# Kernel tuning notes

Hardware: AMD Instinct MI355X
Metric: run time of the kernel (lower is better)

The kernel has to match this reference:

```python
import jax, jax.numpy as jnp
import numpy as np

N = 200_000          # nodes (chain graph)
E = N - 1            # edges = diff structure
F = 5                # node features: [pos, vel_hist(3), cur_vel]
L = 16               # latent_size
G = 2                # globals: [time, static_param]
D = 3 * L + G        # ODE state dim = node_lat + sent_agg + recv_agg + globals
NSTEPS = 4           # fixed RK4 steps standing in for adaptive Tsit5 over t in [0,1]
DT = 0.01            # integrator dt of the physics post-processor


def setup_inputs() -> dict:
    key = jax.random.key(0)
    ks = iter(jax.random.split(key, 32))
    s = 0.1  # small init so the ODE stays well-behaved
    p = lambda shape: jax.random.normal(next(ks), shape, jnp.float32) * s
    inp = {}
    inp["nodes"] = jax.random.normal(next(ks), (N, F), jnp.float32)
    inp["edges"] = jax.random.normal(next(ks), (E, 1), jnp.float32)
    inp["g"] = jnp.zeros((G,), jnp.float32)
    inp["enc_n_w1"] = p((F, L)); inp["enc_n_b1"] = jnp.zeros((L,), jnp.float32)
    inp["enc_n_w2"] = p((L, L)); inp["enc_n_b2"] = jnp.zeros((L,), jnp.float32)
    inp["enc_e_w1"] = p((1, L)); inp["enc_e_b1"] = jnp.zeros((L,), jnp.float32)
    inp["enc_e_w2"] = p((L, L)); inp["enc_e_b2"] = jnp.zeros((L,), jnp.float32)
    inp["ode_w1"] = p((D + 1, D)); inp["ode_b1"] = jnp.zeros((D,), jnp.float32)
    inp["ode_w2"] = p((D, D)); inp["ode_b2"] = jnp.zeros((D,), jnp.float32)
    inp["node_out_w"] = p((D, L)); inp["node_out_b"] = jnp.zeros((L,), jnp.float32)
    inp["dec_n_w1"] = p((L, L)); inp["dec_n_b1"] = jnp.zeros((L,), jnp.float32)
    inp["dec_n_w2"] = p((L, L)); inp["dec_n_b2"] = jnp.zeros((L,), jnp.float32)
    inp["dec_n_w3"] = p((L, 1)); inp["dec_n_b3"] = jnp.zeros((1,), jnp.float32)
    inp["senders"] = jnp.arange(E, dtype=jnp.int32)
    inp["receivers"] = jnp.arange(1, N, dtype=jnp.int32)
    return inp


def reference(nodes, edges, g,
              enc_n_w1, enc_n_b1, enc_n_w2, enc_n_b2,
              enc_e_w1, enc_e_b1, enc_e_w2, enc_e_b2,
              ode_w1, ode_b1, ode_w2, ode_b2,
              node_out_w, node_out_b,
              dec_n_w1, dec_n_b1, dec_n_w2, dec_n_b2, dec_n_w3, dec_n_b3,
              senders, receivers):
    swish = jax.nn.swish
    n = nodes.shape[0]
    cur_pos = nodes[:, 0]
    cur_vel = nodes[:, -1]

    # --- encoder: MLP [L, L] on nodes and edges (swish, no final act) ---
    nlat = swish(nodes @ enc_n_w1 + enc_n_b1) @ enc_n_w2 + enc_n_b2   # [N, L]
    elat = swish(edges @ enc_e_w1 + enc_e_b1) @ enc_e_w2 + enc_e_b2   # [E, L]

    # --- processor (1 MP step): gather/scatter + Neural-ODE node update ---
    sent = jax.ops.segment_sum(elat, senders, num_segments=n)        # [N, L]
    recv = jax.ops.segment_sum(elat, receivers, num_segments=n)      # [N, L]
    gb = jnp.broadcast_to(g, (n, g.shape[0]))                        # [N, G]
    y0 = jnp.concatenate([nlat, sent, recv, gb], axis=1)             # [N, D]

    def f(t, y):  # derivative net: relu MLP on concat(y, t)
        inp = jnp.concatenate([y, jnp.full((y.shape[0], 1), t, y.dtype)], axis=1)
        return jax.nn.relu(inp @ ode_w1 + ode_b1) @ ode_w2 + ode_b2

    h = jnp.float32(1.0 / NSTEPS)

    def step(carry, _):
        y, t = carry
        k1 = f(t, y)
        k2 = f(t + 0.5 * h, y + 0.5 * h * k1)
        k3 = f(t + 0.5 * h, y + 0.5 * h * k2)
        k4 = f(t + h, y + h * k3)
        y = y + (h / 6.0) * (k1 + 2.0 * k2 + 2.0 * k3 + k4)
        return (y, t + h), None

    (yT, _), _ = jax.lax.scan(step, (y0, jnp.float32(0.0)), None, length=NSTEPS)
    nlat2 = yT @ node_out_w + node_out_b                             # [N, L]

    # --- global update: increment time ---
    g_new = jnp.concatenate([g[:1] + 1.0, g[1:]])

    # --- decoder node MLP [L, L, 1] ---
    dh = swish(nlat2 @ dec_n_w1 + dec_n_b1)
    dh = swish(dh @ dec_n_w2 + dec_n_b2)
    pred_acc = (dh @ dec_n_w3 + dec_n_b3).reshape(-1)                # [N]

    # --- semi-implicit Euler post-processor ---
    next_vel = cur_vel + pred_acc * DT
    next_pos = cur_pos + next_vel * DT
    next_nodes = jnp.column_stack([next_pos, nodes[:, 2:], next_vel, pred_acc])
    next_edges = jnp.diff(next_pos).reshape(-1, 1)
    return next_nodes, next_edges, g_new
```

## Files before the change

### kernel.cpp

```cpp
#include <hip/hip_runtime.h>

#define NN 200000
#define EE (NN - 1)
#define NSTEPS 4
#define DTC 0.01f
#define WPB 4
#define NPB 128
#define GRID 1563

typedef __attribute__((ext_vector_type(8))) _Float16 f16x8;
typedef __attribute__((ext_vector_type(2))) _Float16 f16x2;
typedef __attribute__((ext_vector_type(4))) float f32x4;

struct H4 { f16x2 a, b, c, d; };

__device__ __forceinline__ f16x2 c2h(float lo, float hi) {
    return __builtin_bit_cast(f16x2, __builtin_amdgcn_cvt_pkrtz(lo, hi));
}
__device__ __forceinline__ unsigned pk2h(float lo, float hi) {
    return __builtin_bit_cast(unsigned, __builtin_amdgcn_cvt_pkrtz(lo, hi));
}
__device__ __forceinline__ f16x8 h8(f16x2 a, f16x2 b, f16x2 c, f16x2 d) {
    H4 t{a, b, c, d};
    return __builtin_bit_cast(f16x8, t);
}
__device__ __forceinline__ f16x2 relu2(f16x2 v) {
    f16x2 r;
    asm("v_pk_max_f16 %0, %1, 0" : "=v"(r) : "v"(v));
    return r;
}
__device__ __forceinline__ float swishf(float x) { return x / (1.0f + __expf(-x)); }

__device__ __forceinline__ int permk(int k) {
    return (k & 0x23) | ((k & 4) << 2) | ((k & 0x18) >> 1);
}

__device__ __forceinline__ f16x8 setw(f16x8 v, bool cond, unsigned nw) {
    uint4 u = __builtin_bit_cast(uint4, v);
    u.w = cond ? nw : u.w;
    return __builtin_bit_cast(f16x8, u);
}

__global__ void gnode_weights(const float* __restrict__ ode_w1, const float* __restrict__ ode_b1,
                              const float* __restrict__ ode_w2, const float* __restrict__ ode_b2,
                              const float* __restrict__ enc_n_w2, const float* __restrict__ enc_e_w2,
                              const float* __restrict__ dec_n_w1, const float* __restrict__ dec_n_w2,
                              const float* __restrict__ node_out_w,
                              unsigned short* __restrict__ wg)
{
    const int b = blockIdx.x;
    const int tid = threadIdx.x;
    if (b < 8) {
        const int i = tid + b * 256;
        const int od = i >> 5;
        const int k2 = (i & 31) * 2;
        const int s0 = permk(k2);
        const int s1 = s0 + 1;
        float a0 = 0.f, a1 = 0.f, b0 = 0.f, b1 = 0.f;
        if (od < 50) {
            a0 = (s0 <= 50) ? ode_w1[s0 * 50 + od] : 0.f;
            a1 = (s1 <= 50) ? ode_w1[s1 * 50 + od]
                            : ((s1 == 51) ? ode_b1[od] : 0.f);
            b0 = (s0 < 50) ? ode_w2[s0 * 50 + od]
                           : ((s0 == 50) ? ode_b2[od] : 0.f);
            b1 = (s1 < 50) ? ode_w2[s1 * 50 + od] : 0.f;
        }
        const int ct = od >> 4;
        const int mm = od & 15;
        const int kt = k2 >> 5;
        const int qq = (k2 >> 3) & 3;
        const int jj = k2 & 7;
        const int didx = ct * 1024 + kt * 512 + (qq * 16 + mm) * 8 + jj;
        *(unsigned*)(wg + didx) = pk2h(a0, a1);
        *(unsigned*)(wg + 4096 + didx) = pk2h(b0, b1);
    } else if (b < 10) {
        const int i = tid + (b - 8) * 256;
        const int mm = i >> 5;
        const int kp = (i & 31) * 2;
        const int s0 = permk(kp);
        const float v0 = (s0     < 50) ? node_out_w[s0 * 16 + mm] : 0.f;
        const float v1 = (s0 + 1 < 50) ? node_out_w[(s0 + 1) * 16 + mm] : 0.f;
        *(unsigned*)(wg + 10240 + mm * 64 + kp) = pk2h(v0, v1);
    } else {
        const int mm = tid >> 4;
        const int kp = (tid & 15) * 2;
        const bool rl = (kp < 16);
        const float eN0 = rl ? enc_n_w2[kp * 16 + mm] : 0.f;
        const float eN1 = rl ? enc_n_w2[(kp + 1) * 16 + mm] : 0.f;
        const float eE0 = rl ? enc_e_w2[kp * 16 + mm] : 0.f;
        const float eE1 = rl ? enc_e_w2[(kp + 1) * 16 + mm] : 0.f;
        const float d10 = rl ? dec_n_w1[kp * 16 + mm] : 0.f;
        const float d11 = rl ? dec_n_w1[(kp + 1) * 16 + mm] : 0.f;
        const float d20 = rl ? dec_n_w2[kp * 16 + mm] : 0.f;
        const float d21 = rl ? dec_n_w2[(kp + 1) * 16 + mm] : 0.f;
        *(unsigned*)(wg + 8192 + mm * 32 + kp) = pk2h(eN0, eN1);
        *(unsigned*)(wg + 8704 + mm * 32 + kp) = pk2h(eE0, eE1);
        *(unsigned*)(wg + 9216 + mm * 32 + kp) = pk2h(d10, d11);
        *(unsigned*)(wg + 9728 + mm * 32 + kp) = pk2h(d20, d21);
    }
}

__global__ __launch_bounds__(256, 3)
void gnode_main(const float* __restrict__ nodes,
                const float* __restrict__ edges,
                const float* __restrict__ g,
                const float* __restrict__ enc_n_w1, const float* __restrict__ enc_n_b1,
                const float* __restrict__ enc_n_b2,
                const float* __restrict__ enc_e_w1, const float* __restrict__ enc_e_b1,
                const float* __restrict__ enc_e_b2,
                const float* __restrict__ node_out_b,
                const float* __restrict__ dec_n_b1, const float* __restrict__ dec_n_b2,
                const float* __restrict__ dec_n_w3, const float* __restrict__ dec_n_b3,
                const unsigned short* __restrict__ wg,
                float* __restrict__ out, float* __restrict__ npos)
{
    __shared__ __attribute__((aligned(16))) unsigned short dscr[WPB][640];
    __shared__ __attribute__((aligned(16))) unsigned short sw[8192];

    const int tid  = threadIdx.x;
    const int lane = tid & 63;
    const int wave = __builtin_amdgcn_readfirstlane(tid >> 6);
    const int m = lane & 15;
    const int q = lane >> 4;
    const bool q0 = (q == 0);
    unsigned short* const dscrw = &dscr[wave][0];

#pragma unroll
    for (int i = 0; i < 4; ++i)
        ((uint4*)sw)[tid + 256 * i] = ((const uint4*)wg)[tid + 256 * i];

    int nd[2], nc[2];
    nd[0] = blockIdx.x * NPB + wave * 32 + m;
    nd[1] = nd[0] + 16;
    nc[0] = (nd[0] < NN) ? nd[0] : (NN - 1);
    nc[1] = (nd[1] < NN) ? nd[1] : (NN - 1);

    *(uint2*)(dscrw + m * 40 + 16 + q * 4) = make_uint2(0u, 0u);

    const f32x4 zero4 = {0.f, 0.f, 0.f, 0.f};
    const f16x2 h2z = {(_Float16)0.f, (_Float16)0.f};
    const f16x8 z8 = h8(h2z, h2z, h2z, h2z);

    f16x8 Y[2][2], ACC[2][2], A[2][2];

    {
        const f16x8 wNf = *(const f16x8*)(const void*)(wg + 8192 + m * 32 + q * 8);
        const f16x8 wEf = *(const f16x8*)(const void*)(wg + 8704 + m * 32 + q * 8);
        f32x4 bN, bE;
#pragma unroll
        for (int r = 0; r < 4; ++r) { bN[r] = enc_n_b2[q * 4 + r]; bE[r] = enc_e_b2[q * 4 + r]; }
        const float g0v = g[0], g1v = g[1];

#pragma unroll
        for (int tt = 0; tt < 2; ++tt) {
            const int node = nc[tt];
            f32x4 e0, e1, e2;
            {
                float nf[5];
#pragma unroll
                for (int c = 0; c < 5; ++c) nf[c] = nodes[node * 5 + c];
                f16x8 bfr = z8;
                if (q < 2) {
                    float hv[8];
#pragma unroll
                    for (int j = 0; j < 8; ++j) {
                        const int d = q * 8 + j;
                        float s = enc_n_b1[d];
#pragma unroll
                        for (int c = 0; c < 5; ++c) s = fmaf(nf[c], enc_n_w1[c * 16 + d], s);
                        hv[j] = swishf(s);
                    }
                    bfr = h8(c2h(hv[0], hv[1]), c2h(hv[2], hv[3]),
                             c2h(hv[4], hv[5]), c2h(hv[6], hv[7]));
                }
                e0 = __builtin_amdgcn_mfma_f32_16x16x32_f16(wNf, bfr, bN, 0, 0, 0);
            }
            {
                const float ev = (node < EE) ? edges[node] : 0.0f;
                f16x8 bfr = z8;
                if (q < 2) {
                    float hv[8];
#pragma unroll
                    for (int j = 0; j < 8; ++j) {
                        const int d = q * 8 + j;
                        hv[j] = swishf(fmaf(ev, enc_e_w1[d], enc_e_b1[d]));
                    }
                    bfr = h8(c2h(hv[0], hv[1]), c2h(hv[2], hv[3]),
                             c2h(hv[4], hv[5]), c2h(hv[6], hv[7]));
                }
                e1 = __builtin_amdgcn_mfma_f32_16x16x32_f16(wEf, bfr, bE, 0, 0, 0);
                if (node == NN - 1) e1 = zero4;
            }
            {
                const float ev = (node > 0) ? edges[node - 1] : 0.0f;
                f16x8 bfr = z8;
                if (q < 2) {
                    float hv[8];
#pragma unroll
                    for (int j = 0; j < 8; ++j) {
                        const int d = q * 8 + j;
                        hv[j] = swishf(fmaf(ev, enc_e_w1[d], enc_e_b1[d]));
                    }
                    bfr = h8(c2h(hv[0], hv[1]), c2h(hv[2], hv[3]),
                             c2h(hv[4], hv[5]), c2h(hv[6], hv[7]));
                }
                e2 = __builtin_amdgcn_mfma_f32_16x16x32_f16(wEf, bfr, bE, 0, 0, 0);
                if (node == 0) e2 = zero4;
            }
            Y[tt][0] = h8(c2h(e0[0], e0[1]), c2h(e0[2], e0[3]),
                          c2h(e1[0], e1[1]), c2h(e1[2], e1[3]));
            Y[tt][1] = h8(c2h(e2[0], e2[1]), c2h(e2[2], e2[3]),
                          q0 ? c2h(g0v, g1v) : h2z, h2z);
            A[tt][0] = Y[tt][0];
            A[tt][1] = setw(Y[tt][1], q0, pk2h(0.f, 1.f));
        }
    }

    __syncthreads();

    const unsigned short* const swl = sw + (q * 16 + m) * 8;

    const float hh = 1.0f / NSTEPS;
    float t0 = 0.0f;
    const unsigned one2 = 0x3C003C00u;

#pragma clang loop unroll(disable)
    for (int stage = 0; stage < 4 * NSTEPS; ++stage) {
        const int s = stage & 3;

        f32x4 hc[2][4];
#pragma unroll
        for (int ct = 0; ct < 4; ++ct) {
            const f16x8 wa = *(const f16x8*)(const void*)(swl + ct * 1024);
            const f16x8 wb = *(const f16x8*)(const void*)(swl + ct * 1024 + 512);
            f32x4 c0 = __builtin_amdgcn_mfma_f32_16x16x32_f16(wa, A[0][0], zero4, 0, 0, 0);
            f32x4 c1 = __builtin_amdgcn_mfma_f32_16x16x32_f16(wa, A[1][0], zero4, 0, 0, 0);
            hc[0][ct] = __builtin_amdgcn_mfma_f32_16x16x32_f16(wb, A[0][1], c0, 0, 0, 0);
            hc[1][ct] = __builtin_amdgcn_mfma_f32_16x16x32_f16(wb, A[1][1], c1, 0, 0, 0);
        }
        f16x8 H[2][2];
#pragma unroll
        for (int tt = 0; tt < 2; ++tt) {
            H[tt][0] = h8(relu2(c2h(hc[tt][0][0], hc[tt][0][1])),
                          relu2(c2h(hc[tt][0][2], hc[tt][0][3])),
                          relu2(c2h(hc[tt][1][0], hc[tt][1][1])),
                          relu2(c2h(hc[tt][1][2], hc[tt][1][3])));
            f16x8 h1 = h8(relu2(c2h(hc[tt][2][0], hc[tt][2][1])),
                          relu2(c2h(hc[tt][2][2], hc[tt][2][3])),
                          relu2(c2h(hc[tt][3][0], hc[tt][3][1])),
                          relu2(c2h(hc[tt][3][2], hc[tt][3][3])));
            H[tt][1] = setw(h1, q0, one2);
        }
        f32x4 kc[2][4];
#pragma unroll
        for (int ct = 0; ct < 4; ++ct) {
            const f16x8 wa = *(const f16x8*)(const void*)(swl + 4096 + ct * 1024);
            const f16x8 wb = *(const f16x8*)(const void*)(swl + 4096 + ct * 1024 + 512);
            f32x4 c0 = __builtin_amdgcn_mfma_f32_16x16x32_f16(wa, H[0][0], zero4, 0, 0, 0);
            f32x4 c1 = __builtin_amdgcn_mfma_f32_16x16x32_f16(wa, H[1][0], zero4, 0, 0, 0);
            kc[0][ct] = __builtin_amdgcn_mfma_f32_16x16x32_f16(wb, H[0][1], c0, 0, 0, 0);
            kc[1][ct] = __builtin_amdgcn_mfma_f32_16x16x32_f16(wb, H[1][1], c1, 0, 0, 0);
        }

        const float ca = (s == 0 || s == 3) ? hh / 6.0f : hh / 3.0f;
        const float cb = (s == 2) ? hh : 0.5f * hh;
        const f16x2 cah = c2h(ca, ca);
        const f16x2 cbh = c2h(cb, cb);
        const f16x8 ca8 = h8(cah, cah, cah, cah);
        const f16x8 cb8 = h8(cbh, cbh, cbh, cbh);
        float tn;
        if (s < 3) tn = t0 + cb;
        else { t0 += hh; tn = t0; }
        const unsigned tw = pk2h(tn, 1.0f);

#pragma unroll
        for (int tt = 0; tt < 2; ++tt) {
            f16x8 KC0 = h8(c2h(kc[tt][0][0], kc[tt][0][1]), c2h(kc[tt][0][2], kc[tt][0][3]),
                           c2h(kc[tt][1][0], kc[tt][1][1]), c2h(kc[tt][1][2], kc[tt][1][3]));
            f16x8 KC1 = h8(c2h(kc[tt][2][0], kc[tt][2][1]), c2h(kc[tt][2][2], kc[tt][2][3]),
                           c2h(kc[tt][3][0], kc[tt][3][1]), c2h(kc[tt][3][2], kc[tt][3][3]));
            if (s == 0) {
                ACC[tt][0] = ca8 * KC0 + Y[tt][0];
                ACC[tt][1] = ca8 * KC1 + Y[tt][1];
            } else {
                ACC[tt][0] = ca8 * KC0 + ACC[tt][0];
                ACC[tt][1] = ca8 * KC1 + ACC[tt][1];
            }
            f16x8 av0, av1;
            if (s < 3) {
                av0 = cb8 * KC0 + Y[tt][0];
                av1 = cb8 * KC1 + Y[tt][1];
            } else {
                Y[tt][0] = ACC[tt][0];
                Y[tt][1] = ACC[tt][1];
                av0 = ACC[tt][0];
                av1 = ACC[tt][1];
            }
            A[tt][0] = av0;
            A[tt][1] = setw(av1, q0, tw);
        }
    }

    const f16x8 dw1 = *(const f16x8*)(const void*)(wg + 9216 + m * 32 + q * 8);
    const f16x8 dw2 = *(const f16x8*)(const void*)(wg + 9728 + m * 32 + q * 8);
    const f16x8 ow0 = *(const f16x8*)(const void*)(wg + 10240 + m * 64 + q * 8);
    const f16x8 ow1 = *(const f16x8*)(const void*)(wg + 10240 + m * 64 + 32 + q * 8);
    f32x4 bO, bD1, bD2;
    float w3v[4];
#pragma unroll
    for (int r = 0; r < 4; ++r) {
        bO[r]  = node_out_b[q * 4 + r];
        bD1[r] = dec_n_b1[q * 4 + r];
        bD2[r] = dec_n_b2[q * 4 + r];
        w3v[r] = dec_n_w3[q * 4 + r];
    }

#pragma unroll
    for (int tt = 0; tt < 2; ++tt) {
        f32x4 nl2 = __builtin_amdgcn_mfma_f32_16x16x32_f16(ow0, Y[tt][0], bO, 0, 0, 0);
        nl2       = __builtin_amdgcn_mfma_f32_16x16x32_f16(ow1, Y[tt][1], nl2, 0, 0, 0);

        *(uint2*)(dscrw + m * 40 + q * 4) =
            make_uint2(pk2h(nl2[0], nl2[1]), pk2h(nl2[2], nl2[3]));
        f16x8 nB = *(const f16x8*)(const void*)(dscrw + m * 40 + q * 8);
        f32x4 dh = __builtin_amdgcn_mfma_f32_16x16x32_f16(dw1, nB, bD1, 0, 0, 0);
#pragma unroll
        for (int r = 0; r < 4; ++r) dh[r] = swishf(dh[r]);

        *(uint2*)(dscrw + m * 40 + q * 4) =
            make_uint2(pk2h(dh[0], dh[1]), pk2h(dh[2], dh[3]));
        f16x8 dB = *(const f16x8*)(const void*)(dscrw + m * 40 + q * 8);
        f32x4 dh2 = __builtin_amdgcn_mfma_f32_16x16x32_f16(dw2, dB, bD2, 0, 0, 0);
#pragma unroll
        for (int r = 0; r < 4; ++r) dh2[r] = swishf(dh2[r]);

        float p = dh2[0] * w3v[0];
        p = fmaf(dh2[1], w3v[1], p);
        p = fmaf(dh2[2], w3v[2], p);
        p = fmaf(dh2[3], w3v[3], p);
        p += __shfl_xor(p, 16);
        p += __shfl_xor(p, 32);
        p += dec_n_b3[0];

        const int node = nd[tt];
        if (q0 && node < NN) {
            const float cur_pos = nodes[node * 5 + 0];
            const float c2 = nodes[node * 5 + 2];
            const float c3 = nodes[node * 5 + 3];
            const float cur_vel = nodes[node * 5 + 4];
            const float next_vel = fmaf(p, DTC, cur_vel);
            const float next_pos = fmaf(next_vel, DTC, cur_pos);
            out[node * 6 + 0] = next_pos;
            out[node * 6 + 1] = c2;
            out[node * 6 + 2] = c3;
            out[node * 6 + 3] = cur_vel;
            out[node * 6 + 4] = next_vel;
            out[node * 6 + 5] = p;
            npos[node] = next_pos;
        }
    }
}

__global__ void gnode_edges(const float* __restrict__ npos,
                            float* __restrict__ out,
                            const float* __restrict__ g)
{
    const int e = blockIdx.x * blockDim.x + threadIdx.x;
    if (e < EE) {
        out[NN * 6 + e] = npos[e + 1] - npos[e];
    }
    if (e == 0) {
        out[NN * 6 + EE]     = g[0] + 1.0f;
        out[NN * 6 + EE + 1] = g[1];
    }
}

extern "C" void kernel_launch(void* const* d_in, const int* in_sizes, int n_in,
                              void* d_out, int out_size, void* d_ws, size_t ws_size,
                              hipStream_t stream) {
    const float* nodes      = (const float*)d_in[0];
    const float* edges      = (const float*)d_in[1];
    const float* g          = (const float*)d_in[2];
    const float* enc_n_w1   = (const float*)d_in[3];
    const float* enc_n_b1   = (const float*)d_in[4];
    const float* enc_n_w2   = (const float*)d_in[5];
    const float* enc_n_b2   = (const float*)d_in[6];
    const float* enc_e_w1   = (const float*)d_in[7];
    const float* enc_e_b1   = (const float*)d_in[8];
    const float* enc_e_w2   = (const float*)d_in[9];
    const float* enc_e_b2   = (const float*)d_in[10];
    const float* ode_w1     = (const float*)d_in[11];
    const float* ode_b1     = (const float*)d_in[12];
    const float* ode_w2     = (const float*)d_in[13];
    const float* ode_b2     = (const float*)d_in[14];
    const float* node_out_w = (const float*)d_in[15];
    const float* node_out_b = (const float*)d_in[16];
    const float* dec_n_w1   = (const float*)d_in[17];
    const float* dec_n_b1   = (const float*)d_in[18];
    const float* dec_n_w2   = (const float*)d_in[19];
    const float* dec_n_b2   = (const float*)d_in[20];
    const float* dec_n_w3   = (const float*)d_in[21];
    const float* dec_n_b3   = (const float*)d_in[22];
    float* out  = (float*)d_out;
    float* npos = (float*)d_ws;
    unsigned short* wg = (unsigned short*)((char*)d_ws + (size_t)NN * 4);

    gnode_weights<<<11, 256, 0, stream>>>(
        ode_w1, ode_b1, ode_w2, ode_b2,
        enc_n_w2, enc_e_w2, dec_n_w1, dec_n_w2, node_out_w, wg);

    gnode_main<<<GRID, 256, 0, stream>>>(
        nodes, edges, g,
        enc_n_w1, enc_n_b1, enc_n_b2,
        enc_e_w1, enc_e_b1, enc_e_b2,
        node_out_b, dec_n_b1, dec_n_b2, dec_n_w3, dec_n_b3,
        wg, out, npos);

    gnode_edges<<<(EE + 255) / 256, 256, 0, stream>>>(npos, out, g);
}
```

Measured before the change: 169.9 us.

## Exploit linearity of first ODE layer to reuse W1·y across RK4 stages

Computes W1·[y,t] once per RK step and keeps it in fp32, then forms each later stage's pre-activation as that product plus a pre-scaled W1 (by h/2 or h) applied to the previous k, with the time increment injected through a unit entry. This removes the per-stage fp16 construction of y+c·k and lets the accumulate use the stored product. It doubles the shared-memory weight buffer (16K halfs) and adds two pre-scaled weight copies, which may reduce occupancy. The intermediate stage input is no longer rounded to fp16, so numerics shift slightly.

```diff
diff --git a/kernel.cpp b/kernel.cpp
--- a/kernel.cpp
+++ b/kernel.cpp
@@ -50,6 +50,7 @@
 {
     const int b = blockIdx.x;
     const int tid = threadIdx.x;
+    const float hh = 1.0f / NSTEPS;
     if (b < 8) {
         const int i = tid + b * 256;
         const int od = i >> 5;
@@ -71,8 +72,10 @@
         const int qq = (k2 >> 3) & 3;
         const int jj = k2 & 7;
         const int didx = ct * 1024 + kt * 512 + (qq * 16 + mm) * 8 + jj;
-        *(unsigned*)(wg + didx) = pk2h(a0, a1);
-        *(unsigned*)(wg + 4096 + didx) = pk2h(b0, b1);
+        *(unsigned*)(wg + didx)         = pk2h(a0, a1);
+        *(unsigned*)(wg + 4096 + didx)  = pk2h(a0 * (0.5f * hh), a1 * (0.5f * hh));
+        *(unsigned*)(wg + 8192 + didx)  = pk2h(a0 * hh, a1 * hh);
+        *(unsigned*)(wg + 12288 + didx) = pk2h(b0, b1);
     } else if (b < 10) {
         const int i = tid + (b - 8) * 256;
         const int mm = i >> 5;
@@ -80,7 +83,7 @@
         const int s0 = permk(kp);
         const float v0 = (s0     < 50) ? node_out_w[s0 * 16 + mm] : 0.f;
         const float v1 = (s0 + 1 < 50) ? node_out_w[(s0 + 1) * 16 + mm] : 0.f;
-        *(unsigned*)(wg + 10240 + mm * 64 + kp) = pk2h(v0, v1);
+        *(unsigned*)(wg + 18432 + mm * 64 + kp) = pk2h(v0, v1);
     } else {
         const int mm = tid >> 4;
         const int kp = (tid & 15) * 2;
@@ -93,10 +96,10 @@
         const float d11 = rl ? dec_n_w1[(kp + 1) * 16 + mm] : 0.f;
         const float d20 = rl ? dec_n_w2[kp * 16 + mm] : 0.f;
         const float d21 = rl ? dec_n_w2[(kp + 1) * 16 + mm] : 0.f;
-        *(unsigned*)(wg + 8192 + mm * 32 + kp) = pk2h(eN0, eN1);
-        *(unsigned*)(wg + 8704 + mm * 32 + kp) = pk2h(eE0, eE1);
-        *(unsigned*)(wg + 9216 + mm * 32 + kp) = pk2h(d10, d11);
-        *(unsigned*)(wg + 9728 + mm * 32 + kp) = pk2h(d20, d21);
+        *(unsigned*)(wg + 16384 + mm * 32 + kp) = pk2h(eN0, eN1);
+        *(unsigned*)(wg + 16896 + mm * 32 + kp) = pk2h(eE0, eE1);
+        *(unsigned*)(wg + 17408 + mm * 32 + kp) = pk2h(d10, d11);
+        *(unsigned*)(wg + 17920 + mm * 32 + kp) = pk2h(d20, d21);
     }
 }
 
@@ -115,7 +118,7 @@
                 float* __restrict__ out, float* __restrict__ npos)
 {
     __shared__ __attribute__((aligned(16))) unsigned short dscr[WPB][640];
-    __shared__ __attribute__((aligned(16))) unsigned short sw[8192];
+    __shared__ __attribute__((aligned(16))) unsigned short sw[16384];
 
     const int tid  = threadIdx.x;
     const int lane = tid & 63;
@@ -126,7 +129,7 @@
     unsigned short* const dscrw = &dscr[wave][0];
 
 #pragma unroll
-    for (int i = 0; i < 4; ++i)
+    for (int i = 0; i < 8; ++i)
         ((uint4*)sw)[tid + 256 * i] = ((const uint4*)wg)[tid + 256 * i];
 
     int nd[2], nc[2];
@@ -141,11 +144,12 @@
     const f16x2 h2z = {(_Float16)0.f, (_Float16)0.f};
     const f16x8 z8 = h8(h2z, h2z, h2z, h2z);
 
-    f16x8 Y[2][2], ACC[2][2], A[2][2];
+    f16x8 Y[2][2], ACC[2][2], KC[2][2];
+    f32x4 U[2][4];
 
     {
-        const f16x8 wNf = *(const f16x8*)(const void*)(wg + 8192 + m * 32 + q * 8);
-        const f16x8 wEf = *(const f16x8*)(const void*)(wg + 8704 + m * 32 + q * 8);
+        const f16x8 wNf = *(const f16x8*)(const void*)(wg + 16384 + m * 32 + q * 8);
+        const f16x8 wEf = *(const f16x8*)(const void*)(wg + 16896 + m * 32 + q * 8);
         f32x4 bN, bE;
 #pragma unroll
         for (int r = 0; r < 4; ++r) { bN[r] = enc_n_b2[q * 4 + r]; bE[r] = enc_e_b2[q * 4 + r]; }
@@ -211,8 +215,6 @@
                           c2h(e1[0], e1[1]), c2h(e1[2], e1[3]));
             Y[tt][1] = h8(c2h(e2[0], e2[1]), c2h(e2[2], e2[3]),
                           q0 ? c2h(g0v, g1v) : h2z, h2z);
-            A[tt][0] = Y[tt][0];
-            A[tt][1] = setw(Y[tt][1], q0, pk2h(0.f, 1.f));
         }
     }
 
@@ -222,22 +224,39 @@
 
     const float hh = 1.0f / NSTEPS;
     float t0 = 0.0f;
-    const unsigned one2 = 0x3C003C00u;
+    const unsigned inj1 = 0x00003C00u;
 
 #pragma clang loop unroll(disable)
     for (int stage = 0; stage < 4 * NSTEPS; ++stage) {
         const int s = stage & 3;
 
         f32x4 hc[2][4];
-#pragma unroll
-        for (int ct = 0; ct < 4; ++ct) {
-            const f16x8 wa = *(const f16x8*)(const void*)(swl + ct * 1024);
-            const f16x8 wb = *(const f16x8*)(const void*)(swl + ct * 1024 + 512);
-            f32x4 c0 = __builtin_amdgcn_mfma_f32_16x16x32_f16(wa, A[0][0], zero4, 0, 0, 0);
-            f32x4 c1 = __builtin_amdgcn_mfma_f32_16x16x32_f16(wa, A[1][0], zero4, 0, 0, 0);
-            hc[0][ct] = __builtin_amdgcn_mfma_f32_16x16x32_f16(wb, A[0][1], c0, 0, 0, 0);
-            hc[1][ct] = __builtin_amdgcn_mfma_f32_16x16x32_f16(wb, A[1][1], c1, 0, 0, 0);
-        }
+        if (s == 0) {
+#pragma unroll
+            for (int tt = 0; tt < 2; ++tt) {
+                const f16x8 y1x = setw(Y[tt][1], q0, pk2h(t0, 1.0f));
+#pragma unroll
+                for (int ct = 0; ct < 4; ++ct) {
+                    const f16x8 wa = *(const f16x8*)(const void*)(swl + ct * 1024);
+                    const f16x8 wb = *(const f16x8*)(const void*)(swl + ct * 1024 + 512);
+                    f32x4 c0 = __builtin_amdgcn_mfma_f32_16x16x32_f16(wa, Y[tt][0], zero4, 0, 0, 0);
+                    U[tt][ct] = __builtin_amdgcn_mfma_f32_16x16x32_f16(wb, y1x, c0, 0, 0, 0);
+                    hc[tt][ct] = U[tt][ct];
+                }
+            }
+        } else {
+            const int cboff = (s == 3) ? 8192 : 4096;
+#pragma unroll
+            for (int ct = 0; ct < 4; ++ct) {
+                const f16x8 wa = *(const f16x8*)(const void*)(swl + cboff + ct * 1024);
+                const f16x8 wb = *(const f16x8*)(const void*)(swl + cboff + ct * 1024 + 512);
+                f32x4 c0 = __builtin_amdgcn_mfma_f32_16x16x32_f16(wa, KC[0][0], U[0][ct], 0, 0, 0);
+                f32x4 c1 = __builtin_amdgcn_mfma_f32_16x16x32_f16(wa, KC[1][0], U[1][ct], 0, 0, 0);
+                hc[0][ct] = __builtin_amdgcn_mfma_f32_16x16x32_f16(wb, KC[0][1], c0, 0, 0, 0);
+                hc[1][ct] = __builtin_amdgcn_mfma_f32_16x16x32_f16(wb, KC[1][1], c1, 0, 0, 0);
+            }
+        }
+
         f16x8 H[2][2];
 #pragma unroll
         for (int tt = 0; tt < 2; ++tt) {
@@ -249,13 +268,14 @@
                           relu2(c2h(hc[tt][2][2], hc[tt][2][3])),
                           relu2(c2h(hc[tt][3][0], hc[tt][3][1])),
                           relu2(c2h(hc[tt][3][2], hc[tt][3][3])));
-            H[tt][1] = setw(h1, q0, one2);
-        }
+            H[tt][1] = setw(h1, q0, 0x3C003C00u);
+        }
+
         f32x4 kc[2][4];
 #pragma unroll
         for (int ct = 0; ct < 4; ++ct) {
-            const f16x8 wa = *(const f16x8*)(const void*)(swl + 4096 + ct * 1024);
-            const f16x8 wb = *(const f16x8*)(const void*)(swl + 4096 + ct * 1024 + 512);
+            const f16x8 wa = *(const f16x8*)(const void*)(swl + 12288 + ct * 1024);
+            const f16x8 wb = *(const f16x8*)(const void*)(swl + 12288 + ct * 1024 + 512);
             f32x4 c0 = __builtin_amdgcn_mfma_f32_16x16x32_f16(wa, H[0][0], zero4, 0, 0, 0);
             f32x4 c1 = __builtin_amdgcn_mfma_f32_16x16x32_f16(wa, H[1][0], zero4, 0, 0, 0);
             kc[0][ct] = __builtin_amdgcn_mfma_f32_16x16x32_f16(wb, H[0][1], c0, 0, 0, 0);
@@ -263,48 +283,36 @@
         }
 
         const float ca = (s == 0 || s == 3) ? hh / 6.0f : hh / 3.0f;
-        const float cb = (s == 2) ? hh : 0.5f * hh;
         const f16x2 cah = c2h(ca, ca);
-        const f16x2 cbh = c2h(cb, cb);
         const f16x8 ca8 = h8(cah, cah, cah, cah);
-        const f16x8 cb8 = h8(cbh, cbh, cbh, cbh);
-        float tn;
-        if (s < 3) tn = t0 + cb;
-        else { t0 += hh; tn = t0; }
-        const unsigned tw = pk2h(tn, 1.0f);
 
 #pragma unroll
         for (int tt = 0; tt < 2; ++tt) {
-            f16x8 KC0 = h8(c2h(kc[tt][0][0], kc[tt][0][1]), c2h(kc[tt][0][2], kc[tt][0][3]),
+            KC[tt][0] = h8(c2h(kc[tt][0][0], kc[tt][0][1]), c2h(kc[tt][0][2], kc[tt][0][3]),
                            c2h(kc[tt][1][0], kc[tt][1][1]), c2h(kc[tt][1][2], kc[tt][1][3]));
-            f16x8 KC1 = h8(c2h(kc[tt][2][0], kc[tt][2][1]), c2h(kc[tt][2][2], kc[tt][2][3]),
+            KC[tt][1] = h8(c2h(kc[tt][2][0], kc[tt][2][1]), c2h(kc[tt][2][2], kc[tt][2][3]),
                            c2h(kc[tt][3][0], kc[tt][3][1]), c2h(kc[tt][3][2], kc[tt][3][3]));
             if (s == 0) {
-                ACC[tt][0] = ca8 * KC0 + Y[tt][0];
-                ACC[tt][1] = ca8 * KC1 + Y[tt][1];
+                ACC[tt][0] = ca8 * KC[tt][0] + Y[tt][0];
+                ACC[tt][1] = ca8 * KC[tt][1] + Y[tt][1];
             } else {
-                ACC[tt][0] = ca8 * KC0 + ACC[tt][0];
-                ACC[tt][1] = ca8 * KC1 + ACC[tt][1];
-            }
-            f16x8 av0, av1;
+                ACC[tt][0] = ca8 * KC[tt][0] + ACC[tt][0];
+                ACC[tt][1] = ca8 * KC[tt][1] + ACC[tt][1];
+            }
             if (s < 3) {
-                av0 = cb8 * KC0 + Y[tt][0];
-                av1 = cb8 * KC1 + Y[tt][1];
+                KC[tt][1] = setw(KC[tt][1], q0, inj1);
             } else {
                 Y[tt][0] = ACC[tt][0];
                 Y[tt][1] = ACC[tt][1];
-                av0 = ACC[tt][0];
-                av1 = ACC[tt][1];
-            }
-            A[tt][0] = av0;
-            A[tt][1] = setw(av1, q0, tw);
-        }
-    }
-
-    const f16x8 dw1 = *(const f16x8*)(const void*)(wg + 9216 + m * 32 + q * 8);
-    const f16x8 dw2 = *(const f16x8*)(const void*)(wg + 9728 + m * 32 + q * 8);
-    const f16x8 ow0 = *(const f16x8*)(const void*)(wg + 10240 + m * 64 + q * 8);
-    const f16x8 ow1 = *(const f16x8*)(const void*)(wg + 10240 + m * 64 + 32 + q * 8);
+            }
+        }
+        if (s == 3) t0 += hh;
+    }
+
+    const f16x8 dw1 = *(const f16x8*)(const void*)(wg + 17408 + m * 32 + q * 8);
+    const f16x8 dw2 = *(const f16x8*)(const void*)(wg + 17920 + m * 32 + q * 8);
+    const f16x8 ow0 = *(const f16x8*)(const void*)(wg + 18432 + m * 64 + q * 8);
+    const f16x8 ow1 = *(const f16x8*)(const void*)(wg + 18432 + m * 64 + 32 + q * 8);
     f32x4 bO, bD1, bD2;
     float w3v[4];
 #pragma unroll
```

Result: slower. 174.2 us (+2.5%).
